# Kernel tuning notes

Measured on AMD Instinct MI355X. Metric: run time of the kernel, lower is better.

Reference implementation:

```python
import jax, jax.numpy as jnp
import numpy as np

B, T, D, E, K = 4, 1024, 512, 10, 2
H = 4 * D          # expert hidden
CITY, CE = 8, 32   # num cities, city embedding dim
LIN = D + CE + D // 4 + D // 4 + D // 8 + D // 8  # 928 router input dim


def setup_inputs() -> dict:
    key = jax.random.key(0)
    ks = jax.random.split(key, 16)
    s = 0.02  # init scale for weights
    return {
        "x": jax.random.normal(ks[0], (B, T, D), jnp.float32),
        "delta_t": jax.random.normal(ks[1], (B, T, D // 4), jnp.float32),
        "delta_dis": jax.random.normal(ks[2], (B, T, D // 4), jnp.float32),
        "delta_rg": jax.random.normal(ks[3], (B, T, D // 8), jnp.float32),
        "delta_entropy": jax.random.normal(ks[4], (B, T, D // 8), jnp.float32),
        "city_emb": jax.random.normal(ks[5], (CITY, CE), jnp.float32),
        "Wg": jax.random.normal(ks[6], (E, LIN), jnp.float32) * s,
        "bg": jnp.zeros((E,), jnp.float32),
        "Wn": jax.random.normal(ks[7], (E, LIN), jnp.float32) * s,
        "bn": jnp.zeros((E,), jnp.float32),
        "W1": jax.random.normal(ks[8], (E, D, H), jnp.float32) * s,
        "b1": jnp.zeros((E, H), jnp.float32),
        "W2": jax.random.normal(ks[9], (E, H, D), jnp.float32) * s,
        "b2": jnp.zeros((E, D), jnp.float32),
        "noise": jax.random.normal(ks[10], (B, T, E), jnp.float32),
        "city": jax.random.randint(ks[11], (B,), 0, CITY),
    }


def reference(x, delta_t, delta_dis, delta_rg, delta_entropy, city_emb,
              Wg, bg, Wn, bn, W1, b1, W2, b2, noise, city):
    # ---- router: concat features -> noisy top-k gating ----
    ce = city_emb[city]                                   # (B, CE)
    ce = jnp.broadcast_to(ce[:, None, :], (x.shape[0], x.shape[1], ce.shape[-1]))
    h = jnp.concatenate([x, ce, delta_t, delta_dis, delta_rg, delta_entropy], axis=-1)  # (B,T,LIN)
    logits = jnp.einsum('btl,el->bte', h, Wg) + bg        # clean gate logits
    gate1 = jax.nn.softmax(logits, axis=-1)               # dense gate (returned for aux loss)
    noise_logits = jnp.einsum('btl,el->bte', h, Wn) + bn
    noisy = logits + noise * jax.nn.softplus(noise_logits)
    _, idx = jax.lax.top_k(noisy, K)                      # (B,T,K)
    sel = jax.nn.one_hot(idx, E, dtype=noisy.dtype).sum(-2) > 0  # (B,T,E) bool
    gating = jax.nn.softmax(jnp.where(sel, noisy, -jnp.inf), axis=-1)  # zeros off top-k

    # ---- experts: dense compute, combine weighted by sparse gate ----
    flat_x = x.reshape(-1, D)                             # (N, D)
    flat_g = gating.reshape(-1, E)                        # (N, E), zero for non-selected
    hid = jax.nn.gelu(jnp.einsum('nd,edh->neh', flat_x, W1) + b1, approximate=False)
    y = jnp.einsum('neh,ehd->ned', hid, W2) + b2          # (N, E, D)
    out = jnp.einsum('ne,ned->nd', flat_g, y).reshape(x.shape)
    return out, gate1
```

## Files before the change

### kernel.cpp

```cpp
#include <hip/hip_runtime.h>
#include <hip/hip_bf16.h>

#define B_      4
#define T_      1024
#define NTOK    4096
#define D_      512
#define E_      10
#define H_      2048
#define LIN_    928
#define TOPK    2
#define BM      128
#define ROWS_CAP 9472
#define TILES_CAP 74

typedef __bf16 bf16x8 __attribute__((ext_vector_type(8)));
typedef float  f32x4  __attribute__((ext_vector_type(4)));
typedef unsigned short ushort8 __attribute__((ext_vector_type(8)));

#define OFF_W1T   0ull
#define SZ_W1T    (10ull*2048*512*2)
#define OFF_W2T   (OFF_W1T + SZ_W1T)
#define SZ_W2T    SZ_W1T
#define OFF_XG    (OFF_W2T + SZ_W2T)
#define SZ_XG     ((size_t)ROWS_CAP*512*2)
#define OFF_HID   (OFF_XG + SZ_XG)
#define SZ_HID    ((size_t)ROWS_CAP*2048*2)
#define OFF_Y     OFF_W1T
#define OFF_TOKE  (OFF_HID + SZ_HID)
#define OFF_TOKG  (OFF_TOKE + 32768)
#define OFF_TROWS (OFF_TOKG + 32768)
#define OFF_RANK  (OFF_TROWS + 32768)
#define OFF_CNT   (OFF_RANK + 32768)

static __device__ __forceinline__ unsigned short f2b(float f) {
  unsigned int u = __float_as_uint(f);
  unsigned int r = (u + 0x7fffu + ((u >> 16) & 1u)) >> 16;
  return (unsigned short)r;
}

static __device__ __forceinline__ float b2f(unsigned short u) {
  return __uint_as_float(((unsigned int)u) << 16);
}

static __device__ __forceinline__ float gelu_f(float v) {
  float z = fabsf(v) * 0.70710678118654752440f;
  float t = __builtin_amdgcn_rcpf(fmaf(0.3275911f, z, 1.f));
  float p = fmaf(1.061405429f, t, -1.453152027f);
  p = fmaf(p, t, 1.421413741f);
  p = fmaf(p, t, -0.284496736f);
  p = fmaf(p, t, 0.254829592f);
  p = p * t;
  float ex = __expf(-z * z);
  float er = fmaf(-p, ex, 1.f);
  er = (v < 0.f) ? -er : er;
  return 0.5f * v * (1.f + er);
}

static __device__ __forceinline__ void gld16(const void* g, void* l) {
  __builtin_amdgcn_global_load_lds(
      (const __attribute__((address_space(1))) unsigned int*)g,
      (__attribute__((address_space(3))) unsigned int*)l, 16, 0, 0);
}

struct WconvLds { float t[64][129]; };

static __device__ __forceinline__ void wconv_body(
    const float* __restrict__ src, unsigned short* __restrict__ dst,
    int R, int C, int e, int bx, int by, int tid, WconvLds* W) {
  int c0 = bx << 7, r0 = by << 6;
  int rr = tid >> 5, cc4 = (tid & 31) << 2;
  const float* s = src + ((size_t)e * R + r0 + rr) * C + c0 + cc4;
#pragma unroll
  for (int p = 0; p < 8; p++) {
    float4 v = *(const float4*)(s + (size_t)p * 8 * C);
    int row = rr + p * 8;
    W->t[row][cc4 + 0] = v.x; W->t[row][cc4 + 1] = v.y;
    W->t[row][cc4 + 2] = v.z; W->t[row][cc4 + 3] = v.w;
  }
  __syncthreads();
  int rb = (tid & 7) * 8;
#pragma unroll
  for (int p = 0; p < 4; p++) {
    int wc2 = p * 32 + (tid >> 3);
    ushort8 o;
#pragma unroll
    for (int i = 0; i < 8; i++) o[i] = f2b(W->t[rb + i][wc2]);
    *(ushort8*)&dst[((size_t)e * C + c0 + wc2) * R + r0 + rb] = o;
  }
}

__global__ __launch_bounds__(256) void prep_k(
    const float* __restrict__ x, const float* __restrict__ dt,
    const float* __restrict__ dd, const float* __restrict__ dr,
    const float* __restrict__ de, const float* __restrict__ cemb,
    const int* __restrict__ city,
    const float* __restrict__ Wg, const float* __restrict__ Wn,
    const float* __restrict__ W1, const float* __restrict__ W2,
    unsigned short* __restrict__ w1T, unsigned short* __restrict__ w2T,
    float* __restrict__ logits_all) {
  __shared__ WconvLds W;
  int bx = blockIdx.x;
  int tid = threadIdx.x;
  if (bx >= 512) {
    int idx = bx - 512;
    if (idx < 1280) {
      int e = idx >> 7, rem = idx & 127;
      wconv_body(W1, w1T, 512, 2048, e, rem & 15, rem >> 4, tid, &W);
    } else {
      idx -= 1280;
      int e = idx >> 7, rem = idx & 127;
      wconv_body(W2, w2T, 2048, 512, e, rem & 3, rem >> 2, tid, &W);
    }
    return;
  }
  int lane = tid & 63;
  int gw = bx * 4 + (tid >> 6);
  int n0 = gw * 2;
  int cb = city[n0 >> 10];

  float acc[2][20];
#pragma unroll
  for (int j = 0; j < 2; j++)
#pragma unroll
    for (int o = 0; o < 20; o++) acc[j][o] = 0.f;

  {
    float hce = (lane < 32) ? cemb[cb * 32 + lane] : 0.f;
    int c = 512 + (lane & 31);
#pragma unroll
    for (int o = 0; o < 10; o++) {
      float wg = Wg[o * LIN_ + c];
      float wn = Wn[o * LIN_ + c];
#pragma unroll
      for (int j = 0; j < 2; j++) {
        acc[j][o]      = fmaf(hce, wg, acc[j][o]);
        acc[j][10 + o] = fmaf(hce, wn, acc[j][10 + o]);
      }
    }
  }
#pragma unroll
  for (int s = 0; s < 5; s++) {
    const float* hp; int Wd, cofs;
    if      (s == 0) { hp = x;  Wd = 512; cofs = 0;   }
    else if (s == 1) { hp = dt; Wd = 128; cofs = 544; }
    else if (s == 2) { hp = dd; Wd = 128; cofs = 672; }
    else if (s == 3) { hp = dr; Wd = 64;  cofs = 800; }
    else             { hp = de; Wd = 64;  cofs = 864; }
    for (int base = 0; base < Wd; base += 64) {
      int c = cofs + base + lane;
      float wv[20];
#pragma unroll
      for (int o = 0; o < 10; o++) {
        wv[o]      = Wg[o * LIN_ + c];
        wv[10 + o] = Wn[o * LIN_ + c];
      }
      float hv[2];
#pragma unroll
      for (int j = 0; j < 2; j++) hv[j] = hp[(size_t)(n0 + j) * Wd + base + lane];
#pragma unroll
      for (int j = 0; j < 2; j++)
#pragma unroll
        for (int o = 0; o < 20; o++) acc[j][o] = fmaf(hv[j], wv[o], acc[j][o]);
    }
  }
#pragma unroll
  for (int off = 1; off < 64; off <<= 1) {
#pragma unroll
    for (int j = 0; j < 2; j++)
#pragma unroll
      for (int o = 0; o < 20; o++) acc[j][o] += __shfl_xor(acc[j][o], off);
  }
#pragma unroll
  for (int j = 0; j < 2; j++) {
    float v = 0.f;
#pragma unroll
    for (int o = 0; o < 20; o++) if (lane == o) v = acc[j][o];
    if (lane < 20) logits_all[(size_t)(n0 + j) * 20 + lane] = v;
  }
}

__global__ __launch_bounds__(256) void route2_k(
    const float* __restrict__ logits_all,
    const float* __restrict__ bg, const float* __restrict__ bn,
    const float* __restrict__ noise,
    float* __restrict__ gate1, int* __restrict__ tok_e,
    float* __restrict__ tok_g, int* __restrict__ ranks,
    int* __restrict__ counts) {
  __shared__ int lcnt[E_], lbase[E_];
  int tid = threadIdx.x;
  if (tid < E_) lcnt[tid] = 0;
  __syncthreads();
  int n = blockIdx.x * 256 + tid;
  const float* p = &logits_all[(size_t)n * 20];
  float logits[E_], noisy[E_], ex[E_];
  float mx = -3.4e38f;
#pragma unroll
  for (int e = 0; e < E_; e++) { logits[e] = p[e] + bg[e]; mx = fmaxf(mx, logits[e]); }
  float s = 0.f;
#pragma unroll
  for (int e = 0; e < E_; e++) { ex[e] = expf(logits[e] - mx); s += ex[e]; }
  float invs = 1.f / s;
#pragma unroll
  for (int e = 0; e < E_; e++) gate1[(size_t)n * E_ + e] = ex[e] * invs;
#pragma unroll
  for (int e = 0; e < E_; e++) {
    float t = p[10 + e] + bn[e];
    float sp = (t > 20.f) ? t : log1pf(expf(t));
    noisy[e] = logits[e] + noise[(size_t)n * E_ + e] * sp;
  }
  int i0 = 0; float v0 = noisy[0];
#pragma unroll
  for (int e = 1; e < E_; e++) if (noisy[e] > v0) { v0 = noisy[e]; i0 = e; }
  int i1 = -1; float v1 = -3.4e38f;
#pragma unroll
  for (int e = 0; e < E_; e++) if (e != i0 && noisy[e] > v1) { v1 = noisy[e]; i1 = e; }
  float ee = expf(v1 - v0);
  float g0 = 1.f / (1.f + ee);
  tok_e[2 * n] = i0; tok_e[2 * n + 1] = i1;
  tok_g[2 * n] = g0; tok_g[2 * n + 1] = ee * g0;
  int r0 = atomicAdd(&lcnt[i0], 1);
  int r1 = atomicAdd(&lcnt[i1], 1);
  __syncthreads();
  if (tid < E_) lbase[tid] = atomicAdd(&counts[tid], lcnt[tid]);
  __syncthreads();
  ranks[2 * n]     = lbase[i0] + r0;
  ranks[2 * n + 1] = lbase[i1] + r1;
}

__global__ __launch_bounds__(256) void scatgath_k(
    const float* __restrict__ x, const int* __restrict__ tok_e,
    const int* __restrict__ ranks, const int* __restrict__ counts,
    int* __restrict__ token_rows, unsigned short* __restrict__ xg) {
  int n = blockIdx.x * 4 + (threadIdx.x >> 6);
  int lane = threadIdx.x & 63;
  int e0 = tok_e[2 * n], e1 = tok_e[2 * n + 1];
  int off0 = 0, off1 = 0, off = 0;
#pragma unroll
  for (int k = 0; k < E_; k++) {
    if (k == e0) off0 = off;
    if (k == e1) off1 = off;
    off += ((counts[k] + BM - 1) / BM) * BM;
  }
  int p0 = off0 + ranks[2 * n];
  int p1 = off1 + ranks[2 * n + 1];
  if (lane == 0) { token_rows[2 * n] = p0; token_rows[2 * n + 1] = p1; }
  float4 a = *(const float4*)&x[(size_t)n * D_ + lane * 8];
  float4 b = *(const float4*)&x[(size_t)n * D_ + lane * 8 + 4];
  ushort8 o;
  o[0] = f2b(a.x); o[1] = f2b(a.y); o[2] = f2b(a.z); o[3] = f2b(a.w);
  o[4] = f2b(b.x); o[5] = f2b(b.y); o[6] = f2b(b.z); o[7] = f2b(b.w);
  *(ushort8*)&xg[(size_t)p0 * D_ + lane * 8] = o;
  *(ushort8*)&xg[(size_t)p1 * D_ + lane * 8] = o;
}

template<int KD, int ND, int BNT, int GX, int MODE>
__global__ __launch_bounds__(256) void gemm_k(
    const unsigned short* __restrict__ A, const unsigned short* __restrict__ BT,
    const float* __restrict__ bias, unsigned short* __restrict__ outb,
    const int* __restrict__ counts) {
  constexpr int BMT = 128;
  constexpr int WN = BNT / 2;
  constexpr int FN = WN / 16;
  constexpr int PS = (BMT + BNT) / 64;
  constexpr int NT = KD / 32;
  constexpr int BUFSZ = (BMT + BNT) * 32;
  int nwg = GX * TILES_CAP;
  int fid = blockIdx.y * GX + blockIdx.x;
  int w = (fid & 7) * (nwg >> 3) + (fid >> 3);
  int bxs = w % GX, bys = w / GX;
  int e = -1, row0 = 0;
  {
    int off = 0, tt = 0;
#pragma unroll
    for (int k = 0; k < E_; k++) {
      int nt = (counts[k] + BM - 1) / BM;
      if (bys >= tt && bys < tt + nt) { e = k; row0 = off + (bys - tt) * BM; }
      tt += nt; off += nt * BM;
    }
  }
  if (e < 0) return;
  int n0 = bxs * BNT;
  int tid = threadIdx.x;
  int lane = tid & 63, wid = tid >> 6;
  int wr = wid >> 1, wc = wid & 1;
  __shared__ __align__(16) unsigned short LDS[3][BUFSZ];
  f32x4 acc[4][FN] = {};
  const unsigned short* Ab = A + (size_t)row0 * KD;
  const unsigned short* Bb = BT + ((size_t)e * ND + n0) * KD;
  int lrow = lane >> 2, lcol = (lane & 3) * 8;
  int r = lane & 15, g8 = (lane >> 4) * 8;
  const unsigned short* gp[PS];
  int loff[PS];
#pragma unroll
  for (int i = 0; i < PS; i++) {
    int rowb = (wid + 4 * i) * 16;
    gp[i] = (rowb < BMT) ? Ab + (size_t)(rowb + lrow) * KD + lcol
                         : Bb + (size_t)(rowb - BMT + lrow) * KD + lcol;
    loff[i] = rowb * 32;
  }
  auto stage = [&](int buf) {
    unsigned short* lb = &LDS[0][0] + buf * BUFSZ;
#pragma unroll
    for (int i = 0; i < PS; i++) { gld16(gp[i], lb + loff[i]); gp[i] += 32; }
  };
  stage(0); stage(1);
  int cur = 0, nb = 2;
  for (int t = 0; t < NT; ++t) {
    if (t + 2 < NT) {
      stage(nb);
      if constexpr (PS == 4) asm volatile("s_waitcnt vmcnt(8)" ::: "memory");
      else                   asm volatile("s_waitcnt vmcnt(6)" ::: "memory");
    } else if (t + 2 == NT) {
      if constexpr (PS == 4) asm volatile("s_waitcnt vmcnt(4)" ::: "memory");
      else                   asm volatile("s_waitcnt vmcnt(3)" ::: "memory");
    } else {
      asm volatile("s_waitcnt vmcnt(0)" ::: "memory");
    }
    asm volatile("s_barrier" ::: "memory");
    const unsigned short* cb2 = &LDS[0][0] + cur * BUFSZ;
    bf16x8 av[4], bv[FN];
#pragma unroll
    for (int mi = 0; mi < 4; mi++)
      av[mi] = *(const bf16x8*)&cb2[(wr * 64 + mi * 16 + r) * 32 + g8];
#pragma unroll
    for (int ni = 0; ni < FN; ni++)
      bv[ni] = *(const bf16x8*)&cb2[(BMT + wc * WN + ni * 16 + r) * 32 + g8];
#pragma unroll
    for (int mi = 0; mi < 4; mi++)
#pragma unroll
      for (int ni = 0; ni < FN; ni++)
        acc[mi][ni] = __builtin_amdgcn_mfma_f32_16x16x32_bf16(av[mi], bv[ni], acc[mi][ni], 0, 0, 0);
    asm volatile("s_barrier" ::: "memory");
    cur = (cur == 2) ? 0 : cur + 1;
    nb = (nb == 2) ? 0 : nb + 1;
  }
  int rq = (lane >> 4) * 4;
#pragma unroll
  for (int mi = 0; mi < 4; mi++) {
#pragma unroll
    for (int ni = 0; ni < FN; ni++) {
      int col = n0 + wc * WN + ni * 16 + r;
      float bz = (MODE == 0) ? bias[e * ND + col] : 0.f;
#pragma unroll
      for (int q = 0; q < 4; q++) {
        int row = row0 + wr * 64 + mi * 16 + rq + q;
        float v = acc[mi][ni][q];
        if constexpr (MODE == 0) v = gelu_f(v + bz);
        outb[(size_t)row * ND + col] = f2b(v);
      }
    }
  }
}

__global__ void combine_k(const unsigned short* __restrict__ y, const float* __restrict__ b2,
                          const int* __restrict__ token_rows, const int* __restrict__ tok_e,
                          const float* __restrict__ tok_g, float* __restrict__ out) {
  int gid = blockIdx.x * 256 + threadIdx.x;
  int n = gid >> 6;
  int c = (gid & 63) << 3;
  int r0 = token_rows[2 * n], r1 = token_rows[2 * n + 1];
  int e0 = tok_e[2 * n], e1 = tok_e[2 * n + 1];
  float g0 = tok_g[2 * n], g1 = tok_g[2 * n + 1];
  ushort8 y0 = *(const ushort8*)&y[(size_t)r0 * D_ + c];
  ushort8 y1 = *(const ushort8*)&y[(size_t)r1 * D_ + c];
  float ba[8], bb[8], o[8];
  *(float4*)&ba[0] = *(const float4*)&b2[e0 * D_ + c];
  *(float4*)&ba[4] = *(const float4*)&b2[e0 * D_ + c + 4];
  *(float4*)&bb[0] = *(const float4*)&b2[e1 * D_ + c];
  *(float4*)&bb[4] = *(const float4*)&b2[e1 * D_ + c + 4];
#pragma unroll
  for (int j = 0; j < 8; j++)
    o[j] = g0 * (b2f(y0[j]) + ba[j]) + g1 * (b2f(y1[j]) + bb[j]);
  *(float4*)&out[(size_t)n * D_ + c]     = *(float4*)&o[0];
  *(float4*)&out[(size_t)n * D_ + c + 4] = *(float4*)&o[4];
}

extern "C" void kernel_launch(void* const* d_in, const int* in_sizes, int n_in,
                              void* d_out, int out_size, void* d_ws, size_t ws_size,
                              hipStream_t stream) {
  const float* x     = (const float*)d_in[0];
  const float* dt    = (const float*)d_in[1];
  const float* dd    = (const float*)d_in[2];
  const float* dr    = (const float*)d_in[3];
  const float* de    = (const float*)d_in[4];
  const float* cemb  = (const float*)d_in[5];
  const float* Wg    = (const float*)d_in[6];
  const float* bg    = (const float*)d_in[7];
  const float* Wn    = (const float*)d_in[8];
  const float* bn    = (const float*)d_in[9];
  const float* W1    = (const float*)d_in[10];
  const float* b1    = (const float*)d_in[11];
  const float* W2    = (const float*)d_in[12];
  const float* b2    = (const float*)d_in[13];
  const float* noise = (const float*)d_in[14];
  const int*   city  = (const int*)d_in[15];

  float* out   = (float*)d_out;
  float* gate1 = out + (size_t)NTOK * D_;

  char* ws = (char*)d_ws;
  unsigned short* w1T  = (unsigned short*)(ws + OFF_W1T);
  unsigned short* w2T  = (unsigned short*)(ws + OFF_W2T);
  unsigned short* xg   = (unsigned short*)(ws + OFF_XG);
  unsigned short* hid  = (unsigned short*)(ws + OFF_HID);
  unsigned short* yb16 = (unsigned short*)(ws + OFF_Y);
  int*    tok_e       = (int*)(ws + OFF_TOKE);
  float*  tok_g       = (float*)(ws + OFF_TOKG);
  int*    token_rows  = (int*)(ws + OFF_TROWS);
  int*    ranks       = (int*)(ws + OFF_RANK);
  int*    counts      = (int*)(ws + OFF_CNT);
  float*  logits_all  = (float*)(ws + OFF_HID);

  hipMemsetAsync(counts, 0, E_ * sizeof(int), stream);
  prep_k<<<3072, 256, 0, stream>>>(x, dt, dd, dr, de, cemb, city, Wg, Wn,
                                   W1, W2, w1T, w2T, logits_all);
  route2_k<<<16, 256, 0, stream>>>(logits_all, bg, bn, noise, gate1, tok_e, tok_g,
                                   ranks, counts);
  scatgath_k<<<1024, 256, 0, stream>>>(x, tok_e, ranks, counts, token_rows, xg);
  gemm_k<512, 2048, 128, 16, 0><<<dim3(16, TILES_CAP), 256, 0, stream>>>(xg, w1T, b1, hid, counts);
  gemm_k<2048, 512, 64, 8, 1><<<dim3(8, TILES_CAP), 256, 0, stream>>>(hid, w2T, nullptr, yb16, counts);
  combine_k<<<1024, 256, 0, stream>>>(yb16, b2, token_rows, tok_e, tok_g, out);
}
```

Measured before the change: 127.9 us.

## Split-K the down-projection GEMM into two halves with wider N tiles

The second expert GEMM (K=2048) now runs as two K-halves of 1024 along a new grid z dimension. It uses 128-wide N tiles instead of 64, so each block gets more data reuse while the total block count stays the same. Each half writes its own bf16 partial output buffer, and the combine kernel reads and sums both partials before applying bias and gates. This adds extra partial-output traffic and an extra bf16 rounding of the partial sums. It also requires the workspace region for y to hold two ROWS_CAP×D slices.

```diff
diff --git a/kernel.cpp b/kernel.cpp
--- a/kernel.cpp
+++ b/kernel.cpp
@@ -253,21 +253,25 @@
   *(ushort8*)&xg[(size_t)p1 * D_ + lane * 8] = o;
 }
 
-template<int KD, int ND, int BNT, int GX, int MODE>
+template<int KD, int ND, int BNT, int GX, int KS, int MODE>
 __global__ __launch_bounds__(256) void gemm_k(
     const unsigned short* __restrict__ A, const unsigned short* __restrict__ BT,
     const float* __restrict__ bias, unsigned short* __restrict__ outb,
     const int* __restrict__ counts) {
+  constexpr int KFULL = KD * KS;
   constexpr int BMT = 128;
   constexpr int WN = BNT / 2;
   constexpr int FN = WN / 16;
   constexpr int PS = (BMT + BNT) / 64;
   constexpr int NT = KD / 32;
   constexpr int BUFSZ = (BMT + BNT) * 32;
-  int nwg = GX * TILES_CAP;
-  int fid = blockIdx.y * GX + blockIdx.x;
+  int nwg = GX * TILES_CAP * KS;
+  int fid = (blockIdx.z * TILES_CAP + blockIdx.y) * GX + blockIdx.x;
   int w = (fid & 7) * (nwg >> 3) + (fid >> 3);
-  int bxs = w % GX, bys = w / GX;
+  int bxs = w % GX;
+  int rem = w / GX;
+  int bys = rem % TILES_CAP;
+  int ks  = rem / TILES_CAP;
   int e = -1, row0 = 0;
   {
     int off = 0, tt = 0;
@@ -285,8 +289,8 @@
   int wr = wid >> 1, wc = wid & 1;
   __shared__ __align__(16) unsigned short LDS[3][BUFSZ];
   f32x4 acc[4][FN] = {};
-  const unsigned short* Ab = A + (size_t)row0 * KD;
-  const unsigned short* Bb = BT + ((size_t)e * ND + n0) * KD;
+  const unsigned short* Ab = A + (size_t)row0 * KFULL + (size_t)ks * KD;
+  const unsigned short* Bb = BT + ((size_t)e * ND + n0) * KFULL + (size_t)ks * KD;
   int lrow = lane >> 2, lcol = (lane & 3) * 8;
   int r = lane & 15, g8 = (lane >> 4) * 8;
   const unsigned short* gp[PS];
@@ -294,8 +298,8 @@
 #pragma unroll
   for (int i = 0; i < PS; i++) {
     int rowb = (wid + 4 * i) * 16;
-    gp[i] = (rowb < BMT) ? Ab + (size_t)(rowb + lrow) * KD + lcol
-                         : Bb + (size_t)(rowb - BMT + lrow) * KD + lcol;
+    gp[i] = (rowb < BMT) ? Ab + (size_t)(rowb + lrow) * KFULL + lcol
+                         : Bb + (size_t)(rowb - BMT + lrow) * KFULL + lcol;
     loff[i] = rowb * 32;
   }
   auto stage = [&](int buf) {
@@ -308,11 +312,9 @@
   for (int t = 0; t < NT; ++t) {
     if (t + 2 < NT) {
       stage(nb);
-      if constexpr (PS == 4) asm volatile("s_waitcnt vmcnt(8)" ::: "memory");
-      else                   asm volatile("s_waitcnt vmcnt(6)" ::: "memory");
+      asm volatile("s_waitcnt vmcnt(8)" ::: "memory");
     } else if (t + 2 == NT) {
-      if constexpr (PS == 4) asm volatile("s_waitcnt vmcnt(4)" ::: "memory");
-      else                   asm volatile("s_waitcnt vmcnt(3)" ::: "memory");
+      asm volatile("s_waitcnt vmcnt(4)" ::: "memory");
     } else {
       asm volatile("s_waitcnt vmcnt(0)" ::: "memory");
     }
@@ -334,6 +336,7 @@
     cur = (cur == 2) ? 0 : cur + 1;
     nb = (nb == 2) ? 0 : nb + 1;
   }
+  unsigned short* outp = outb + (size_t)ks * ROWS_CAP * ND;
   int rq = (lane >> 4) * 4;
 #pragma unroll
   for (int mi = 0; mi < 4; mi++) {
@@ -346,7 +349,7 @@
         int row = row0 + wr * 64 + mi * 16 + rq + q;
         float v = acc[mi][ni][q];
         if constexpr (MODE == 0) v = gelu_f(v + bz);
-        outb[(size_t)row * ND + col] = f2b(v);
+        outp[(size_t)row * ND + col] = f2b(v);
       }
     }
   }
@@ -355,14 +358,17 @@
 __global__ void combine_k(const unsigned short* __restrict__ y, const float* __restrict__ b2,
                           const int* __restrict__ token_rows, const int* __restrict__ tok_e,
                           const float* __restrict__ tok_g, float* __restrict__ out) {
+  const unsigned short* yB = y + (size_t)ROWS_CAP * D_;
   int gid = blockIdx.x * 256 + threadIdx.x;
   int n = gid >> 6;
   int c = (gid & 63) << 3;
   int r0 = token_rows[2 * n], r1 = token_rows[2 * n + 1];
   int e0 = tok_e[2 * n], e1 = tok_e[2 * n + 1];
   float g0 = tok_g[2 * n], g1 = tok_g[2 * n + 1];
-  ushort8 y0 = *(const ushort8*)&y[(size_t)r0 * D_ + c];
-  ushort8 y1 = *(const ushort8*)&y[(size_t)r1 * D_ + c];
+  ushort8 y0a = *(const ushort8*)&y [(size_t)r0 * D_ + c];
+  ushort8 y0b = *(const ushort8*)&yB[(size_t)r0 * D_ + c];
+  ushort8 y1a = *(const ushort8*)&y [(size_t)r1 * D_ + c];
+  ushort8 y1b = *(const ushort8*)&yB[(size_t)r1 * D_ + c];
   float ba[8], bb[8], o[8];
   *(float4*)&ba[0] = *(const float4*)&b2[e0 * D_ + c];
   *(float4*)&ba[4] = *(const float4*)&b2[e0 * D_ + c + 4];
@@ -370,7 +376,8 @@
   *(float4*)&bb[4] = *(const float4*)&b2[e1 * D_ + c + 4];
 #pragma unroll
   for (int j = 0; j < 8; j++)
-    o[j] = g0 * (b2f(y0[j]) + ba[j]) + g1 * (b2f(y1[j]) + bb[j]);
+    o[j] = g0 * (b2f(y0a[j]) + b2f(y0b[j]) + ba[j]) +
+           g1 * (b2f(y1a[j]) + b2f(y1b[j]) + bb[j]);
   *(float4*)&out[(size_t)n * D_ + c]     = *(float4*)&o[0];
   *(float4*)&out[(size_t)n * D_ + c + 4] = *(float4*)&o[4];
 }
@@ -417,7 +424,7 @@
   route2_k<<<16, 256, 0, stream>>>(logits_all, bg, bn, noise, gate1, tok_e, tok_g,
                                    ranks, counts);
   scatgath_k<<<1024, 256, 0, stream>>>(x, tok_e, ranks, counts, token_rows, xg);
-  gemm_k<512, 2048, 128, 16, 0><<<dim3(16, TILES_CAP), 256, 0, stream>>>(xg, w1T, b1, hid, counts);
-  gemm_k<2048, 512, 64, 8, 1><<<dim3(8, TILES_CAP), 256, 0, stream>>>(hid, w2T, nullptr, yb16, counts);
+  gemm_k<512, 2048, 128, 16, 1, 0><<<dim3(16, TILES_CAP, 1), 256, 0, stream>>>(xg, w1T, b1, hid, counts);
+  gemm_k<1024, 512, 128, 4, 2, 1><<<dim3(4, TILES_CAP, 2), 256, 0, stream>>>(hid, w2T, nullptr, yb16, counts);
   combine_k<<<1024, 256, 0, stream>>>(yb16, b2, token_rows, tok_e, tok_g, out);
 }
```

After: 121.8 us. 4.8% less time.
